# Optimization experiments

Hardware: AMD Instinct MI355X
Metric: run time of the kernel (lower is better)

## Reference

```python
import jax, jax.numpy as jnp
import numpy as np

ZH_DIMS = 512
ZH_HID = 1024
ZH_VOC = 32000
EN_HID = 512
B = 64
L = 32
EN_LEN = 40


def setup_inputs() -> dict:
    key = jax.random.key(0)
    ks = jax.random.split(key, 10)
    s = 0.02
    return {
        "sent_inputs": jax.random.normal(ks[0], (B, L, ZH_DIMS), dtype=jnp.float32),
        "hidden_state": jax.random.normal(ks[1], (B, EN_LEN, EN_HID), dtype=jnp.float32),
        "W_ih": jax.random.normal(ks[2], (4 * ZH_HID, ZH_DIMS), dtype=jnp.float32) * s,
        "W_hh": jax.random.normal(ks[3], (4 * ZH_HID, ZH_HID), dtype=jnp.float32) * s,
        "b_ih": jax.random.normal(ks[4], (4 * ZH_HID,), dtype=jnp.float32) * s,
        "b_hh": jax.random.normal(ks[5], (4 * ZH_HID,), dtype=jnp.float32) * s,
        "W_p": jax.random.normal(ks[6], (ZH_HID, EN_HID), dtype=jnp.float32) * s,
        "b_p": jax.random.normal(ks[7], (ZH_HID,), dtype=jnp.float32) * s,
        "W_v": jax.random.normal(ks[8], (ZH_VOC, ZH_HID), dtype=jnp.float32) * s,
        "b_v": jax.random.normal(ks[9], (ZH_VOC,), dtype=jnp.float32) * s,
    }


def reference(sent_inputs, hidden_state, W_ih, W_hh, b_ih, b_hh, W_p, b_p, W_v, b_v):
    # hx from last encoder step, projected en_hidden -> zh_hidden (sizes differ)
    hx = hidden_state[:, -1, :] @ W_p.T + b_p          # [B, H]
    cx = jnp.zeros_like(hx)                            # [B, H]
    xs = jnp.swapaxes(sent_inputs, 0, 1)               # [L, B, D]

    def step(carry, x):
        hx, cx = carry
        gates = x @ W_ih.T + b_ih + hx @ W_hh.T + b_hh  # [B, 4H]
        i, f, g, o = jnp.split(gates, 4, axis=-1)       # PyTorch LSTMCell gate order
        cx_new = jax.nn.sigmoid(f) * cx + jax.nn.sigmoid(i) * jnp.tanh(g)
        hx_new = jax.nn.sigmoid(o) * jnp.tanh(cx_new)
        logit = hx_new @ W_v.T + b_v                    # [B, V]
        return (hx_new, cx_new), logit

    _, logits = jax.lax.scan(step, (hx, cx), xs)        # logits: [L, B, V]
    predicts = jnp.argmax(logits, axis=-1).astype(jnp.float32)  # [L, B]
    return jnp.swapaxes(logits, 0, 1), predicts.T
```

## Files before the change

### kernel.cpp

```cpp
#include <hip/hip_runtime.h>
#include <hip/hip_cooperative_groups.h>

namespace cg = cooperative_groups;

#define BB 64
#define LL 32
#define DD 512
#define HH 1024
#define GG 4096
#define VV 32000
#define EHH 512
#define ELL 40

#define OFF_H   0
#define OFF_HT  (33*BB*HH)
#define OFF_RM  (OFF_HT + 2*HH*BB)
#define OFF_GX  (OFF_RM + 2048)

typedef __attribute__((ext_vector_type(8))) short bf16x8;
typedef __attribute__((ext_vector_type(4))) float f32x4;

__device__ __forceinline__ unsigned long long packkey(float v, int n) {
    unsigned u = __float_as_uint(v);
    u = (u & 0x80000000u) ? ~u : (u | 0x80000000u);
    return ((unsigned long long)u << 32) | (unsigned)(0x7FFFFFFF - n);
}
__device__ __forceinline__ unsigned key32(float v) {
    unsigned u = __float_as_uint(v);
    return (u & 0x80000000u) ? ~u : (u | 0x80000000u);
}
__device__ __forceinline__ float keyinv(unsigned k) {
    unsigned u = (k & 0x80000000u) ? (k & 0x7FFFFFFFu) : ~k;
    return __uint_as_float(u);
}
__device__ __forceinline__ unsigned short f2bf(float v) {
    unsigned u = __float_as_uint(v);
    return (unsigned short)((u + 0x7FFFu + ((u >> 16) & 1u)) >> 16);
}
__device__ __forceinline__ float bf2f(unsigned short b) {
    return __uint_as_float(((unsigned)b) << 16);
}

__global__ __launch_bounds__(128) void init_kernel(
    const float* __restrict__ hid, const float* __restrict__ Wp,
    const float* __restrict__ bp, float* __restrict__ hst,
    float* __restrict__ hT, unsigned* __restrict__ rowmax)
{
    int b = blockIdx.x;
    int h = blockIdx.y * 128 + threadIdx.x;
    const float4* hrow = (const float4*)(hid + ((size_t)b*ELL + (ELL-1))*EHH);
    const float4* wrow = (const float4*)(Wp + (size_t)h*EHH);
    float acc = 0.f;
    #pragma unroll 4
    for (int k = 0; k < EHH/4; ++k) {
        float4 a = hrow[k], w = wrow[k];
        acc += a.x*w.x + a.y*w.y + a.z*w.z + a.w*w.w;
    }
    float v = acc + bp[h];
    hst[(size_t)b*HH + h] = v;
    hT[(size_t)h*BB + b] = v;
    int tg = (b*8 + blockIdx.y)*128 + threadIdx.x;
    if (tg < LL*BB) rowmax[tg] = 0u;
}

__global__ __launch_bounds__(256) void whhT_kernel(
    const float* __restrict__ W, float* __restrict__ WT)
{
    __shared__ float t[64][65];
    const int bx = blockIdx.x;
    const int by = blockIdx.y;
    const int tid = threadIdx.x;
    const int c4 = (tid & 15) * 4, rr = tid >> 4;
    #pragma unroll
    for (int p = 0; p < 4; ++p) {
        int r = p*16 + rr;
        float4 v = *(const float4*)(W + ((size_t)(bx*64 + r))*HH + by*64 + c4);
        t[r][c4+0] = v.x; t[r][c4+1] = v.y; t[r][c4+2] = v.z; t[r][c4+3] = v.w;
    }
    __syncthreads();
    #pragma unroll
    for (int p = 0; p < 4; ++p) {
        int k = p*16 + rr;
        float4 o;
        o.x = t[c4+0][k]; o.y = t[c4+1][k]; o.z = t[c4+2][k]; o.w = t[c4+3][k];
        *(float4*)(WT + ((size_t)(by*64 + k))*GG + bx*64 + c4) = o;
    }
}

#define KT 16
__global__ __launch_bounds__(256) void gates_x_kernel(
    const float* __restrict__ x, const float* __restrict__ Wih,
    const float* __restrict__ bih, const float* __restrict__ bhh,
    float* __restrict__ gxT)
{
    __shared__ float As[KT][68];
    __shared__ float Bs[KT][68];
    const int l  = blockIdx.x;
    const int n0 = blockIdx.y * 64;
    const int tid = threadIdx.x;
    const int tx = tid & 15, ty = tid >> 4;
    float acc[4][4] = {};
    for (int k0 = 0; k0 < DD; k0 += KT) {
        int i = tid * 4;
        int m = i >> 4, kk = i & 15;
        float4 a = *(const float4*)(Wih + (size_t)(n0+m)*DD + k0 + kk);
        As[kk+0][m]=a.x; As[kk+1][m]=a.y; As[kk+2][m]=a.z; As[kk+3][m]=a.w;
        float4 w = *(const float4*)(x + ((size_t)m*LL + l)*DD + k0 + kk);
        Bs[kk+0][m]=w.x; Bs[kk+1][m]=w.y; Bs[kk+2][m]=w.z; Bs[kk+3][m]=w.w;
        __syncthreads();
        #pragma unroll
        for (int k = 0; k < KT; ++k) {
            float4 av = *(const float4*)&As[k][ty*4];
            float4 bv = *(const float4*)&Bs[k][tx*4];
            float aa[4] = {av.x,av.y,av.z,av.w};
            float bb2[4] = {bv.x,bv.y,bv.z,bv.w};
            #pragma unroll
            for (int i2 = 0; i2 < 4; ++i2)
                #pragma unroll
                for (int j = 0; j < 4; ++j)
                    acc[i2][j] += aa[i2]*bb2[j];
        }
        __syncthreads();
    }
    #pragma unroll
    for (int i2 = 0; i2 < 4; ++i2) {
        int g = n0 + ty*4 + i2;
        float bias = bih[g] + bhh[g];
        float4 o;
        o.x = acc[i2][0] + bias;
        o.y = acc[i2][1] + bias;
        o.z = acc[i2][2] + bias;
        o.w = acc[i2][3] + bias;
        *(float4*)(gxT + ((size_t)l*GG + g)*BB + tx*4) = o;
    }
}

__global__ __launch_bounds__(1024) void lstm_persist_kernel(
    const float* __restrict__ gxT,
    const float* __restrict__ WT,
    float* __restrict__ hst,
    float* __restrict__ hT)
{
    extern __shared__ float Gs[];
    const int w = blockIdx.x;
    const int h0 = w*4;
    const int tid = threadIdx.x;
    const int wid = tid >> 6;
    const int lane = tid & 63;
    const int gq = lane >> 4;
    const int b0 = (lane & 15) * 4;

    float c = 0.f;
    cg::grid_group grid = cg::this_grid();

    for (int s = 1; s <= LL; ++s) {
        const float* hprev = hT + (((s-1)&1) ? (HH*BB) : 0);
        float gxv0=0.f, gxv1=0.f, gxv2=0.f, gxv3=0.f;
        if (wid < 4) {
            const float* gp = gxT + ((size_t)(s-1)*GG + h0 + wid)*BB + lane;
            gxv0 = gp[0*HH*BB];
            gxv1 = gp[1*HH*BB];
            gxv2 = gp[2*HH*BB];
            gxv3 = gp[3*HH*BB];
        }
        f32x4 a0 = {0,0,0,0}, a1 = {0,0,0,0}, a2 = {0,0,0,0}, a3 = {0,0,0,0};
        {
            const float* hp = hprev + (size_t)(wid*64)*BB + b0;
            const float* wp = WT + (size_t)(wid*64)*GG + gq*HH + h0;
            #pragma unroll 8
            for (int k = 0; k < 64; ++k) {
                float4 hv = *(const float4*)(hp + (size_t)k*BB);
                float4 wv = *(const float4*)(wp + (size_t)k*GG);
                a0.x += wv.x*hv.x; a0.y += wv.x*hv.y; a0.z += wv.x*hv.z; a0.w += wv.x*hv.w;
                a1.x += wv.y*hv.x; a1.y += wv.y*hv.y; a1.z += wv.y*hv.z; a1.w += wv.y*hv.w;
                a2.x += wv.z*hv.x; a2.y += wv.z*hv.y; a2.z += wv.z*hv.z; a2.w += wv.z*hv.w;
                a3.x += wv.w*hv.x; a3.y += wv.w*hv.y; a3.z += wv.w*hv.z; a3.w += wv.w*hv.w;
            }
        }
        *(f32x4*)&Gs[(((gq*4+0)*16) + wid)*64 + b0] = a0;
        *(f32x4*)&Gs[(((gq*4+1)*16) + wid)*64 + b0] = a1;
        *(f32x4*)&Gs[(((gq*4+2)*16) + wid)*64 + b0] = a2;
        *(f32x4*)&Gs[(((gq*4+3)*16) + wid)*64 + b0] = a3;
        __syncthreads();
        if (wid < 4) {
            int j = wid, b = lane;
            float gacc[4] = {gxv0, gxv1, gxv2, gxv3};
            #pragma unroll
            for (int g = 0; g < 4; ++g) {
                const float* q = Gs + (size_t)((g*4 + j)*16)*64 + b;
                float sum = 0.f;
                #pragma unroll
                for (int kh = 0; kh < 16; ++kh) sum += q[kh*64];
                gacc[g] += sum;
            }
            float si = 1.f/(1.f + expf(-gacc[0]));
            float sf = 1.f/(1.f + expf(-gacc[1]));
            float so = 1.f/(1.f + expf(-gacc[3]));
            float cn = sf*c + si*tanhf(gacc[2]);
            float hn = so*tanhf(cn);
            c = cn;
            int h = h0 + j;
            hst[((size_t)s*BB + b)*HH + h] = hn;
            float* hTn = hT + ((s&1) ? (HH*BB) : 0);
            hTn[(size_t)h*BB + b] = hn;
        }
        grid.sync();
    }
}

__global__ __launch_bounds__(256) void hsplit_kernel(
    const float* __restrict__ hs, unsigned short* __restrict__ Ahi,
    unsigned short* __restrict__ Alo)
{
    int t = blockIdx.x*256 + threadIdx.x;
    int row = t >> 7, ko = (t & 127) << 3;
    const float* src = hs + (size_t)row*HH + ko;
    float4 f0 = *(const float4*)(src);
    float4 f1 = *(const float4*)(src + 4);
    float vs[8] = {f0.x,f0.y,f0.z,f0.w,f1.x,f1.y,f1.z,f1.w};
    union { bf16x8 v; unsigned short u[8]; } hi, lo;
    #pragma unroll
    for (int e = 0; e < 8; ++e) {
        unsigned short h = f2bf(vs[e]);
        hi.u[e] = h;
        lo.u[e] = f2bf(vs[e] - bf2f(h));
    }
    size_t off = ((((size_t)(row>>4)*32 + (ko>>5))*64) + ((ko&31)>>3)*16 + (row&15))*8;
    *(bf16x8*)(Ahi + off) = hi.v;
    *(bf16x8*)(Alo + off) = lo.v;
}

__global__ __launch_bounds__(256, 2) void logits_mfma_kernel(
    const unsigned short* __restrict__ Ahi, const unsigned short* __restrict__ Alo,
    const float* __restrict__ Wv, const float* __restrict__ bv,
    float* __restrict__ out, unsigned* __restrict__ rowmax)
{
    __shared__ bf16x8 Bhi[4][128];
    __shared__ bf16x8 Blo[4][128];
    const int rb = blockIdx.x;
    const int cb = blockIdx.y;
    const int n0 = cb*128;
    const int tid = threadIdx.x;
    const int wid = tid >> 6, lane = tid & 63;
    const int wy = wid >> 1, wx = wid & 1;
    const int l15 = lane & 15, l4 = lane >> 4;
    f32x4 acc[4][4] = {};

    const int sc = tid >> 1, skh = tid & 1;
    const float* wsrc = Wv + (size_t)(n0 + sc)*HH + skh*16;
    const size_t abase = (size_t)(rb*8 + wy*4)*32;

    for (int ks = 0; ks < 32; ++ks) {
        float4 f0 = *(const float4*)(wsrc + ks*32);
        float4 f1 = *(const float4*)(wsrc + ks*32 + 4);
        float4 f2 = *(const float4*)(wsrc + ks*32 + 8);
        float4 f3 = *(const float4*)(wsrc + ks*32 + 12);
        __syncthreads();
        {
            float va[8] = {f0.x,f0.y,f0.z,f0.w,f1.x,f1.y,f1.z,f1.w};
            float vb[8] = {f2.x,f2.y,f2.z,f2.w,f3.x,f3.y,f3.z,f3.w};
            union { bf16x8 v; unsigned short u[8]; } h0, l0, h1, l1;
            #pragma unroll
            for (int e = 0; e < 8; ++e) {
                unsigned short ha = f2bf(va[e]);
                h0.u[e] = ha; l0.u[e] = f2bf(va[e] - bf2f(ha));
                unsigned short hb = f2bf(vb[e]);
                h1.u[e] = hb; l1.u[e] = f2bf(vb[e] - bf2f(hb));
            }
            Bhi[skh*2+0][sc] = h0.v;  Blo[skh*2+0][sc] = l0.v;
            Bhi[skh*2+1][sc] = h1.v;  Blo[skh*2+1][sc] = l1.v;
        }
        __syncthreads();
        bf16x8 ah[4], al[4], bh[4], bl[4];
        #pragma unroll
        for (int mf = 0; mf < 4; ++mf) {
            size_t o = ((abase + (size_t)mf*32 + ks)*64 + lane)*8;
            ah[mf] = *(const bf16x8*)(Ahi + o);
            al[mf] = *(const bf16x8*)(Alo + o);
        }
        #pragma unroll
        for (int nf = 0; nf < 4; ++nf) {
            int cc = wx*64 + nf*16 + l15;
            bh[nf] = Bhi[l4][cc];
            bl[nf] = Blo[l4][cc];
        }
        #pragma unroll
        for (int mf = 0; mf < 4; ++mf)
            #pragma unroll
            for (int nf = 0; nf < 4; ++nf) {
                acc[mf][nf] = __builtin_amdgcn_mfma_f32_16x16x32_bf16(ah[mf], bh[nf], acc[mf][nf], 0,0,0);
                acc[mf][nf] = __builtin_amdgcn_mfma_f32_16x16x32_bf16(ah[mf], bl[nf], acc[mf][nf], 0,0,0);
                acc[mf][nf] = __builtin_amdgcn_mfma_f32_16x16x32_bf16(al[mf], bh[nf], acc[mf][nf], 0,0,0);
            }
    }
    unsigned rk[4][4];
    #pragma unroll
    for (int mf = 0; mf < 4; ++mf)
        #pragma unroll
        for (int j = 0; j < 4; ++j) rk[mf][j] = 0u;
    #pragma unroll
    for (int mf = 0; mf < 4; ++mf) {
        int rowg = rb*128 + wy*64 + mf*16 + l4*4;
        #pragma unroll
        for (int nf = 0; nf < 4; ++nf) {
            int col = n0 + wx*64 + nf*16 + l15;
            float bvv = bv[col];
            #pragma unroll
            for (int j = 0; j < 4; ++j) {
                float v = acc[mf][nf][j] + bvv;
                int row = rowg + j;
                int b = row & 63, l = row >> 6;
                out[((size_t)b*LL + l)*VV + col] = v;
                unsigned key = key32(v);
                if (key > rk[mf][j]) rk[mf][j] = key;
            }
        }
    }
    #pragma unroll
    for (int o = 1; o < 16; o <<= 1)
        #pragma unroll
        for (int mf = 0; mf < 4; ++mf)
            #pragma unroll
            for (int j = 0; j < 4; ++j) {
                unsigned t = __shfl_xor(rk[mf][j], o);
                if (t > rk[mf][j]) rk[mf][j] = t;
            }
    if (l15 == 0) {
        #pragma unroll
        for (int mf = 0; mf < 4; ++mf)
            #pragma unroll
            for (int j = 0; j < 4; ++j)
                atomicMax(&rowmax[rb*128 + wy*64 + mf*16 + l4*4 + j], rk[mf][j]);
    }
}

__global__ __launch_bounds__(256) void argmax_kernel(
    const float* __restrict__ out, const unsigned* __restrict__ rowmax,
    const float* __restrict__ hs, const float* __restrict__ Wv,
    const float* __restrict__ bv, float* __restrict__ pred)
{
    const int r = blockIdx.x;
    const int b = r & 63, l = r >> 6;
    const int tid = threadIdx.x;
    const float* row = out + ((size_t)b*LL + l)*VV;
    const float thr = keyinv(rowmax[r]) - 2e-3f;
    __shared__ int cnt;
    __shared__ int cand[32];
    __shared__ float ps[4];
    if (tid == 0) cnt = 0;
    __syncthreads();
    for (int i = tid*4; i < VV; i += 1024) {
        float4 v = *(const float4*)(row + i);
        if (v.x >= thr) { int p = atomicAdd(&cnt,1); if (p < 32) cand[p] = i; }
        if (v.y >= thr) { int p = atomicAdd(&cnt,1); if (p < 32) cand[p] = i+1; }
        if (v.z >= thr) { int p = atomicAdd(&cnt,1); if (p < 32) cand[p] = i+2; }
        if (v.w >= thr) { int p = atomicAdd(&cnt,1); if (p < 32) cand[p] = i+3; }
    }
    __syncthreads();
    int nc = cnt < 32 ? cnt : 32;
    unsigned long long best = 0ULL;
    const float* hrow = hs + (size_t)r*HH;
    float4 a = *(const float4*)(hrow + tid*4);
    for (int ci = 0; ci < nc; ++ci) {
        int n = cand[ci];
        float4 wv = *(const float4*)(Wv + (size_t)n*HH + tid*4);
        float p = a.x*wv.x + a.y*wv.y + a.z*wv.z + a.w*wv.w;
        #pragma unroll
        for (int o = 1; o < 64; o <<= 1) p += __shfl_xor(p, o);
        if ((tid & 63) == 0) ps[tid >> 6] = p;
        __syncthreads();
        if (tid == 0) {
            float tot = ps[0] + ps[1] + ps[2] + ps[3] + bv[n];
            unsigned long long k2 = packkey(tot, n);
            if (k2 > best) best = k2;
        }
        __syncthreads();
    }
    if (tid == 0)
        pred[b*LL + l] = (float)(0x7FFFFFFFu - (unsigned)(best & 0xFFFFFFFFu));
}

extern "C" void kernel_launch(void* const* d_in, const int* in_sizes, int n_in,
                              void* d_out, int out_size, void* d_ws, size_t ws_size,
                              hipStream_t stream) {
    (void)in_sizes; (void)n_in; (void)out_size; (void)ws_size;
    const float* sent = (const float*)d_in[0];
    const float* hid  = (const float*)d_in[1];
    const float* Wih  = (const float*)d_in[2];
    const float* Whh  = (const float*)d_in[3];
    const float* bih  = (const float*)d_in[4];
    const float* bhh  = (const float*)d_in[5];
    const float* Wp   = (const float*)d_in[6];
    const float* bp   = (const float*)d_in[7];
    const float* Wv   = (const float*)d_in[8];
    const float* bv   = (const float*)d_in[9];
    float* out = (float*)d_out;

    float* ws  = (float*)d_ws;
    float* hst = ws + OFF_H;
    float* hT  = ws + OFF_HT;
    unsigned* rowmax = (unsigned*)(ws + OFF_RM);
    float* gxT = ws + OFF_GX;
    unsigned short* Ahi = (unsigned short*)(ws + OFF_GX);
    unsigned short* Alo = Ahi + (size_t)2048*HH;

    float* WT = out;

    init_kernel<<<dim3(BB, 8), 128, 0, stream>>>(hid, Wp, bp, hst, hT, rowmax);
    whhT_kernel<<<dim3(GG/64, HH/64), 256, 0, stream>>>(Whh, WT);
    gates_x_kernel<<<dim3(LL, GG/64), 256, 0, stream>>>(sent, Wih, bih, bhh, gxT);

    {
        const float* gxp = gxT;
        const float* WTp = WT;
        float* hstp = hst;
        float* hTp = hT;
        void* kargs[] = { (void*)&gxp, (void*)&WTp, (void*)&hstp, (void*)&hTp };
        hipLaunchCooperativeKernel((void*)lstm_persist_kernel, dim3(256), dim3(1024),
                                   kargs, 16*16*64*sizeof(float), stream);
    }

    hsplit_kernel<<<dim3(1024), 256, 0, stream>>>(hst + (size_t)BB*HH, Ahi, Alo);
    logits_mfma_kernel<<<dim3(16, VV/128), 256, 0, stream>>>(Ahi, Alo, Wv, bv, out, rowmax);
    argmax_kernel<<<dim3(LL*BB), 256, 0, stream>>>(
        out, rowmax, hst + (size_t)BB*HH, Wv, bv, out + (size_t)BB*LL*VV);
}
```

Baseline: 2.818 ms.

## Keep each block's W_hh slice resident in LDS inside the persistent LSTM kernel

Removes the separate W_hh transpose kernel. Each persistent block now loads its 16 rows of W_hh (4 hidden units × 4 gates × 1024) once into shared memory in transposed layout and reuses it across all 32 timesteps. Previously those weights were re-read from global/L2 every step. This costs 128KB of LDS per block, which could limit occupancy and needs the larger dynamic shared allocation to fit. The LDS writes during the load are strided and may cause bank conflicts.

```diff
diff --git a/kernel.cpp b/kernel.cpp
--- a/kernel.cpp
+++ b/kernel.cpp
@@ -61,30 +61,6 @@
     hT[(size_t)h*BB + b] = v;
     int tg = (b*8 + blockIdx.y)*128 + threadIdx.x;
     if (tg < LL*BB) rowmax[tg] = 0u;
-}
-
-__global__ __launch_bounds__(256) void whhT_kernel(
-    const float* __restrict__ W, float* __restrict__ WT)
-{
-    __shared__ float t[64][65];
-    const int bx = blockIdx.x;
-    const int by = blockIdx.y;
-    const int tid = threadIdx.x;
-    const int c4 = (tid & 15) * 4, rr = tid >> 4;
-    #pragma unroll
-    for (int p = 0; p < 4; ++p) {
-        int r = p*16 + rr;
-        float4 v = *(const float4*)(W + ((size_t)(bx*64 + r))*HH + by*64 + c4);
-        t[r][c4+0] = v.x; t[r][c4+1] = v.y; t[r][c4+2] = v.z; t[r][c4+3] = v.w;
-    }
-    __syncthreads();
-    #pragma unroll
-    for (int p = 0; p < 4; ++p) {
-        int k = p*16 + rr;
-        float4 o;
-        o.x = t[c4+0][k]; o.y = t[c4+1][k]; o.z = t[c4+2][k]; o.w = t[c4+3][k];
-        *(float4*)(WT + ((size_t)(by*64 + k))*GG + bx*64 + c4) = o;
-    }
 }
 
 #define KT 16
@@ -137,11 +113,13 @@
 
 __global__ __launch_bounds__(1024) void lstm_persist_kernel(
     const float* __restrict__ gxT,
-    const float* __restrict__ WT,
+    const float* __restrict__ Whh,
     float* __restrict__ hst,
     float* __restrict__ hT)
 {
-    extern __shared__ float Gs[];
+    extern __shared__ float smem[];
+    float* Ws = smem;
+    float* Gs = smem + 16384;
     const int w = blockIdx.x;
     const int h0 = w*4;
     const int tid = threadIdx.x;
@@ -150,8 +128,23 @@
     const int gq = lane >> 4;
     const int b0 = (lane & 15) * 4;
 
+    {
+        int rr = tid >> 6;
+        int g = rr >> 2, j = rr & 3;
+        const float* src = Whh + ((size_t)(g*HH + h0 + j))*HH;
+        int kbase = (tid & 63) * 4;
+        #pragma unroll
+        for (int cch = 0; cch < 4; ++cch) {
+            float4 v = *(const float4*)(src + kbase + cch*256);
+            Ws[(kbase + cch*256 + 0)*16 + rr] = v.x;
+            Ws[(kbase + cch*256 + 1)*16 + rr] = v.y;
+            Ws[(kbase + cch*256 + 2)*16 + rr] = v.z;
+            Ws[(kbase + cch*256 + 3)*16 + rr] = v.w;
+        }
+    }
     float c = 0.f;
     cg::grid_group grid = cg::this_grid();
+    __syncthreads();
 
     for (int s = 1; s <= LL; ++s) {
         const float* hprev = hT + (((s-1)&1) ? (HH*BB) : 0);
@@ -166,11 +159,11 @@
         f32x4 a0 = {0,0,0,0}, a1 = {0,0,0,0}, a2 = {0,0,0,0}, a3 = {0,0,0,0};
         {
             const float* hp = hprev + (size_t)(wid*64)*BB + b0;
-            const float* wp = WT + (size_t)(wid*64)*GG + gq*HH + h0;
+            const float* wp = Ws + (wid*64)*16 + gq*4;
             #pragma unroll 8
             for (int k = 0; k < 64; ++k) {
                 float4 hv = *(const float4*)(hp + (size_t)k*BB);
-                float4 wv = *(const float4*)(wp + (size_t)k*GG);
+                float4 wv = *(const float4*)(wp + k*16);
                 a0.x += wv.x*hv.x; a0.y += wv.x*hv.y; a0.z += wv.x*hv.z; a0.w += wv.x*hv.w;
                 a1.x += wv.y*hv.x; a1.y += wv.y*hv.y; a1.z += wv.y*hv.z; a1.w += wv.y*hv.w;
                 a2.x += wv.z*hv.x; a2.y += wv.z*hv.y; a2.z += wv.z*hv.z; a2.w += wv.z*hv.w;
@@ -404,20 +397,17 @@
     unsigned short* Ahi = (unsigned short*)(ws + OFF_GX);
     unsigned short* Alo = Ahi + (size_t)2048*HH;
 
-    float* WT = out;
-
     init_kernel<<<dim3(BB, 8), 128, 0, stream>>>(hid, Wp, bp, hst, hT, rowmax);
-    whhT_kernel<<<dim3(GG/64, HH/64), 256, 0, stream>>>(Whh, WT);
     gates_x_kernel<<<dim3(LL, GG/64), 256, 0, stream>>>(sent, Wih, bih, bhh, gxT);
 
     {
         const float* gxp = gxT;
-        const float* WTp = WT;
+        const float* Whhp = Whh;
         float* hstp = hst;
         float* hTp = hT;
-        void* kargs[] = { (void*)&gxp, (void*)&WTp, (void*)&hstp, (void*)&hTp };
+        void* kargs[] = { (void*)&gxp, (void*)&Whhp, (void*)&hstp, (void*)&hTp };
         hipLaunchCooperativeKernel((void*)lstm_persist_kernel, dim3(256), dim3(1024),
-                                   kargs, 16*16*64*sizeof(float), stream);
+                                   kargs, 2*16384*sizeof(float), stream);
     }
 
     hsplit_kernel<<<dim3(1024), 256, 0, stream>>>(hst + (size_t)BB*HH, Ahi, Alo);
```

Measured after the change: 2.404 ms. -14.7%, faster.
